# Performance work log

Hardware: AMD Instinct MI355X
Metric: run time of the kernel (lower is better)

## Reference

```python
import jax, jax.numpy as jnp
import numpy as np

N = 20000      # nodes per set
E = 320000     # edges per graph (avg degree 16)
C = 256        # embed_channels
H = 4          # num_heads
D = C // H     # head dim
P = 3          # pos_dim


def setup_inputs() -> dict:
    key = jax.random.key(0)
    ks = jax.random.split(key, 16)
    f32 = jnp.float32
    rn = lambda k, s, sc=1.0: jax.random.normal(k, s, dtype=f32) * sc
    ri = lambda k: jax.random.randint(k, (2, E), 0, N, dtype=jnp.int32)
    return {
        "feat1": rn(ks[0], (N, C)),
        "coord1": rn(ks[1], (N, P)),
        "feat2": rn(ks[2], (N, C)),
        "coord2": rn(ks[3], (N, P)),
        "Wqkv1": rn(ks[4], (C, 6 * C), 0.02),
        "bqkv1": jnp.zeros((6 * C,), f32),
        "Wqkv2": rn(ks[5], (C, 6 * C), 0.02),
        "bqkv2": jnp.zeros((6 * C,), f32),
        "Wproj1": rn(ks[6], (2 * C, C), 0.02),
        "bproj1": jnp.zeros((C,), f32),
        "Wproj2": rn(ks[7], (2 * C, C), 0.02),
        "bproj2": jnp.zeros((C,), f32),
        "Wrpe": rn(ks[8], (P, C), 0.02),
        "brpe": jnp.zeros((C,), f32),
        "graph1": ri(ks[9]),
        "graph2": ri(ks[10]),
        "graph12": ri(ks[11]),
        "graph21": ri(ks[12]),
    }


def _edge_attention(key_, query, value, g, n, rpe=None):
    # key_/query/value: [n_src_or_dst, H, D]; g: [2, E]; rpe: [E, H, D] or None
    k = key_[g[1]]          # [E, H, D] gather source
    q = query[g[0]]         # [E, H, D] gather destination
    v = value[g[1]]         # [E, H, D]
    s = k * q
    if rpe is not None:
        s = s + rpe
    s = s.sum(-1)           # [E, H] per-edge, per-head score
    dst = g[0]
    m = jax.ops.segment_max(s, dst, num_segments=n)      # [n, H]
    e = jnp.exp(s - m[dst])
    z = jax.ops.segment_sum(e, dst, num_segments=n)      # [n, H]
    a = e / z[dst]                                       # scatter-softmax
    out = jax.ops.segment_sum(a[..., None] * v, dst, num_segments=n)  # [n, H, D]
    return out.reshape(n, H * D)


def _qkv(feat, W, b):
    n = feat.shape[0]
    qkv = (feat @ W + b).reshape(n, 6, H, D)
    return tuple(qkv[:, i] for i in range(6))  # q_a,k_a,v_a,q_b,k_b,v_b


def reference(feat1, coord1, feat2, coord2, Wqkv1, bqkv1, Wqkv2, bqkv2,
              Wproj1, bproj1, Wproj2, bproj2, Wrpe, brpe,
              graph1, graph2, graph12, graph21):
    n1, n2 = feat1.shape[0], feat2.shape[0]
    q11, k11, v11, q12, k12, v12 = _qkv(feat1, Wqkv1, bqkv1)
    q21, k21, v21, q22, k22, v22 = _qkv(feat2, Wqkv2, bqkv2)

    rpe1 = ((coord1[graph1[0]] - coord1[graph1[1]]) @ Wrpe + brpe).reshape(-1, H, D)
    rpe2 = ((coord2[graph2[0]] - coord2[graph2[1]]) @ Wrpe + brpe).reshape(-1, H, D)

    feat11 = _edge_attention(k11, q11, v11, graph1, n1, rpe1)
    feat22 = _edge_attention(k22, q22, v22, graph2, n2, rpe2)
    feat12 = _edge_attention(k21, q12, v21, graph21, n1)
    feat21 = _edge_attention(k12, q21, v12, graph12, n2)

    out1 = jnp.concatenate([feat11, feat12], axis=1) @ Wproj1 + bproj1
    out2 = jnp.concatenate([feat22, feat21], axis=1) @ Wproj2 + bproj2
    return (out1, out2)
```

## Files before the change

kernel.cpp:

```cpp
#include <hip/hip_runtime.h>
#include <stdint.h>
#include <stddef.h>

#define N_NODES 20000
#define N_EDGES 320000

typedef unsigned short u16;
typedef __attribute__((ext_vector_type(8))) short bf16x8;
typedef __attribute__((ext_vector_type(8))) unsigned short u16x8;
typedef __attribute__((ext_vector_type(4))) float f32x4;

__device__ __forceinline__ float bf2f(u16 u) {
    union { unsigned int i; float f; } v; v.i = ((unsigned int)u) << 16; return v.f;
}
__device__ __forceinline__ u16 f2bf(float f) {
    union { float f; unsigned int i; } v; v.f = f;
    unsigned int x = v.i;
    unsigned int r = x + 0x7fffu + ((x >> 16) & 1u);
    return (u16)(r >> 16);
}
__device__ __forceinline__ int clampi(int v, int lo, int hi) {
    return v < lo ? lo : (v > hi ? hi : v);
}
__device__ __forceinline__ float ld1(const void* p, size_t i, int f32) {
    return f32 ? ((const float*)p)[i] : bf2f(((const u16*)p)[i]);
}

__device__ __forceinline__ void async_ld16(void* lds, const void* g) {
    __builtin_amdgcn_global_load_lds(
        (const __attribute__((address_space(1))) unsigned int*)g,
        (__attribute__((address_space(3))) unsigned int*)lds,
        16, 0, 0);
}

__device__ __forceinline__ int xcd_chunk(int b, int nwg) {
    int x = b & 7, idx = b >> 3;
    int q = nwg >> 3, r = nwg & 7;
    return ((x < r) ? (x * (q + 1)) : (r * (q + 1) + (x - r) * q)) + idx;
}

__global__ void marker_kernel(u16* out, u16 code) { out[threadIdx.x] = code; }

__global__ void detect_kernel(const void* feat, int* diag) {
    int lane = threadIdx.x;
    int weird = 0;
    const u16* p = (const u16*)feat;
    for (int i = lane; i < 512; i += 64) {
        float v = bf2f(p[i]);
        float a = fabsf(v);
        if (!(a <= 1e4f) || (a != 0.f && a < 1e-6f)) weird++;
    }
#pragma unroll
    for (int off = 32; off > 0; off >>= 1) weird += __shfl_xor(weird, off, 64);
    if (lane == 0) { diag[0] = 123456; diag[1] = (weird > 51) ? 1 : 0; diag[2] = 0; }
}

__global__ void rpe_sums_kernel(const void* __restrict__ Wrpe, const void* __restrict__ brpe,
                                float* __restrict__ out, const int* __restrict__ dflag) {
    int f32 = dflag[0];
    int t = threadIdx.x;
    if (t < 12) {
        int p = t >> 2, h = t & 3;
        float s = 0.f;
        for (int d = 0; d < 64; ++d) s += ld1(Wrpe, p * 256 + h * 64 + d, f32);
        out[t] = s;
    } else if (t < 16) {
        int h = t - 12;
        float s = 0.f;
        for (int d = 0; d < 64; ++d) s += ld1(brpe, h * 64 + d, f32);
        out[12 + h] = s;
    }
}

__global__ __launch_bounds__(256) void coordproj_kernel(const void* __restrict__ coord,
                                                        const int* __restrict__ dflag,
                                                        const float* __restrict__ rs,
                                                        float* __restrict__ proj, int n) {
    int i = blockIdx.x * 256 + threadIdx.x;
    if (i >= n * 4) return;
    int f32 = dflag[0];
    int node = i >> 2, h = i & 3;
    float s = ld1(coord, (size_t)node * 3 + 0, f32) * rs[0 * 4 + h]
            + ld1(coord, (size_t)node * 3 + 1, f32) * rs[1 * 4 + h]
            + ld1(coord, (size_t)node * 3 + 2, f32) * rs[2 * 4 + h];
    proj[i] = s;
}

__global__ __launch_bounds__(256) void transpose_w_kernel(const void* __restrict__ W,
                                                          const int* __restrict__ dflag,
                                                          u16* __restrict__ Wt, int K, int N) {
    int f32 = dflag[0];
    int i = blockIdx.x * 256 + threadIdx.x;
    if (i >= K * N) return;
    int n = i / K, k = i - n * K;
    Wt[i] = f2bf(ld1(W, (size_t)k * N + n, f32));
}

__global__ __launch_bounds__(256) void tobf16_kernel(
        const void* __restrict__ a, const void* __restrict__ b,
        const int* __restrict__ dflag, u16* __restrict__ oa, u16* __restrict__ ob) {
    const int PER = N_NODES * 256 / 8;
    int idx = blockIdx.x * 256 + threadIdx.x;
    if (idx >= 2 * PER) return;
    int set = idx >= PER;
    int j = (idx - set * PER) * 8;
    const void* src = set ? b : a;
    u16* dst = set ? ob : oa;
    int f32 = dflag[0];
    u16x8 o;
    if (f32) {
        const float* p = (const float*)src + j;
        float4 u0 = *(const float4*)p, u1 = *(const float4*)(p + 4);
        o[0] = f2bf(u0.x); o[1] = f2bf(u0.y); o[2] = f2bf(u0.z); o[3] = f2bf(u0.w);
        o[4] = f2bf(u1.x); o[5] = f2bf(u1.y); o[6] = f2bf(u1.z); o[7] = f2bf(u1.w);
    } else {
        o = *(const u16x8*)((const u16*)src + j);
    }
    *(u16x8*)(dst + j) = o;
}

__global__ __launch_bounds__(256) void count_kernel(
        const int* __restrict__ g0, const int* __restrict__ g1,
        const int* __restrict__ g2, const int* __restrict__ g3,
        int* __restrict__ deg, u16* __restrict__ rank) {
    int b = blockIdx.x;
    int gi = b & 3;
    int h = (b >> 2) & 1;
    int e = (b >> 2) * 256 + (int)threadIdx.x;
    if (e >= N_EDGES) return;
    const int* g = (gi == 0) ? g0 : (gi == 1) ? g1 : (gi == 2) ? g2 : g3;
    int dst = clampi(g[e], 0, N_NODES - 1);
    int pos = atomicAdd(&deg[(gi * 2 + h) * N_NODES + dst], 1);
    pos = pos & 0x7fff;
    rank[(size_t)gi * N_EDGES + e] = (u16)((h << 15) | pos);
}

__global__ __launch_bounds__(256) void scan_kernel(const int* __restrict__ cur,
                                                   int* __restrict__ rowptr) {
    int g = blockIdx.x;
    int tid = threadIdx.x;
    __shared__ int buf[256];
    const int* d0 = cur + (g * 2 + 0) * N_NODES;
    const int* d1 = cur + (g * 2 + 1) * N_NODES;
    int* rp = rowptr + g * (N_NODES + 1);
    const int CH = (N_NODES + 255) / 256;
    int lo = tid * CH;
    int hi = lo + CH; if (hi > N_NODES) hi = N_NODES;
    int s = 0;
    for (int i = lo; i < hi; ++i) s += d0[i] + d1[i];
    buf[tid] = s;
    __syncthreads();
    for (int off = 1; off < 256; off <<= 1) {
        int x = (tid >= off) ? buf[tid - off] : 0;
        __syncthreads();
        buf[tid] += x;
        __syncthreads();
    }
    int run = (tid == 0) ? 0 : buf[tid - 1];
    for (int i = lo; i < hi; ++i) {
        rp[i] = run;
        run += d0[i] + d1[i];
    }
    if (tid == 255) rp[N_NODES] = buf[255];
}

__global__ __launch_bounds__(256) void fill_kernel(
        const int* __restrict__ g0, const int* __restrict__ g1,
        const int* __restrict__ g2, const int* __restrict__ g3,
        const int* __restrict__ rowptr, const int* __restrict__ cur,
        const u16* __restrict__ rank, u16* __restrict__ col) {
    int b = blockIdx.x;
    int gi = b & 3;
    int e = (b >> 2) * 256 + (int)threadIdx.x;
    if (e >= N_EDGES) return;
    const int* g = (gi == 0) ? g0 : (gi == 1) ? g1 : (gi == 2) ? g2 : g3;
    int dst = clampi(g[e], 0, N_NODES - 1);
    int src = clampi(g[N_EDGES + e], 0, N_NODES - 1);
    u16 rk = rank[(size_t)gi * N_EDGES + e];
    int h = rk >> 15, r = rk & 0x7fff;
    int base = h ? cur[(gi * 2 + 0) * N_NODES + dst] : 0;
    int pos = rowptr[gi * (N_NODES + 1) + dst] + base + r;
    if (pos >= 0 && pos < N_EDGES)
        col[(size_t)gi * N_EDGES + pos] = (u16)src;
}

__global__ __launch_bounds__(256) void gemm_mfma(
        const void* __restrict__ A, int lda, const int* __restrict__ aflag,
        const u16* __restrict__ Bt,
        const void* __restrict__ bias, size_t biasoff, const int* __restrict__ bflag,
        void* __restrict__ C, size_t coff, int ldc, const int* __restrict__ cflag,
        int M, int N, int K) {
    __shared__ __align__(16) u16 As[128 * 40];
    __shared__ __align__(16) u16 Bs[128 * 40];
    const int f32a = aflag[0], f32b = bflag[0], f32c = cflag[0];
    const int t = threadIdx.x;
    const int lane = t & 63, wv = t >> 6;
    const int wm = (wv >> 1) * 64, wn = (wv & 1) * 64;
    const int m0 = blockIdx.y * 128, n0 = blockIdx.x * 128;
    const int l15 = lane & 15, lq = lane >> 4;

    f32x4 acc[4][4];
#pragma unroll
    for (int i = 0; i < 4; ++i)
#pragma unroll
        for (int j = 0; j < 4; ++j) acc[i][j] = (f32x4){0.f, 0.f, 0.f, 0.f};

    const int sr = t >> 1, skc = (t & 1) * 16;

    for (int k0 = 0; k0 < K; k0 += 32) {
        __syncthreads();
        {
            __align__(16) u16 tmp[16];
            int gm = m0 + sr;
            if (gm < M) {
                if (f32a) {
                    const float* ap = (const float*)A + (size_t)gm * lda + k0 + skc;
#pragma unroll
                    for (int i = 0; i < 16; i += 4) {
                        float4 u = *(const float4*)(ap + i);
                        tmp[i] = f2bf(u.x); tmp[i + 1] = f2bf(u.y);
                        tmp[i + 2] = f2bf(u.z); tmp[i + 3] = f2bf(u.w);
                    }
                } else {
                    const u16* ap = (const u16*)A + (size_t)gm * lda + k0 + skc;
                    *(u16x8*)&tmp[0] = *(const u16x8*)ap;
                    *(u16x8*)&tmp[8] = *(const u16x8*)(ap + 8);
                }
            } else {
#pragma unroll
                for (int i = 0; i < 16; ++i) tmp[i] = 0;
            }
            *(u16x8*)&As[sr * 40 + skc] = *(u16x8*)&tmp[0];
            *(u16x8*)&As[sr * 40 + skc + 8] = *(u16x8*)&tmp[8];
        }
        {
            const u16* bp = Bt + (size_t)(n0 + sr) * K + k0 + skc;
            u16x8 b0 = *(const u16x8*)bp;
            u16x8 b1 = *(const u16x8*)(bp + 8);
            *(u16x8*)&Bs[sr * 40 + skc] = b0;
            *(u16x8*)&Bs[sr * 40 + skc + 8] = b1;
        }
        __syncthreads();
        bf16x8 af[4], bfr[4];
#pragma unroll
        for (int mt = 0; mt < 4; ++mt)
            af[mt] = *(const bf16x8*)&As[(wm + mt * 16 + l15) * 40 + lq * 8];
#pragma unroll
        for (int nt = 0; nt < 4; ++nt)
            bfr[nt] = *(const bf16x8*)&Bs[(wn + nt * 16 + l15) * 40 + lq * 8];
#pragma unroll
        for (int mt = 0; mt < 4; ++mt)
#pragma unroll
            for (int nt = 0; nt < 4; ++nt)
                acc[mt][nt] = __builtin_amdgcn_mfma_f32_16x16x32_bf16(af[mt], bfr[nt], acc[mt][nt], 0, 0, 0);
    }
#pragma unroll
    for (int mt = 0; mt < 4; ++mt) {
#pragma unroll
        for (int nt = 0; nt < 4; ++nt) {
            int gn = n0 + wn + nt * 16 + l15;
            float bb = ld1(bias, biasoff + gn, f32b);
#pragma unroll
            for (int r = 0; r < 4; ++r) {
                int gm = m0 + wm + mt * 16 + lq * 4 + r;
                if (gm < M) {
                    float v = acc[mt][nt][r] + bb;
                    size_t ic = coff + (size_t)gm * ldc + gn;
                    if (f32c) ((float*)C)[ic] = v;
                    else      ((u16*)C)[ic] = f2bf(v);
                }
            }
        }
    }
}

__global__ __launch_bounds__(256, 4) void gemm_pipe(
        const u16* __restrict__ A1, const u16* __restrict__ A2, int K,
        const u16* __restrict__ Bt1, const u16* __restrict__ Bt2,
        const void* __restrict__ bias1, const void* __restrict__ bias2,
        const int* __restrict__ bflag,
        void* __restrict__ C, size_t coff1, size_t coff2, int ldc,
        const int* __restrict__ cflag,
        int M, int nr, int nc) {
    __shared__ __align__(16) u16 S[16384];
    u16* As = S;
    u16* Bs = S + 8192;
    const int f32b = bflag[0], f32c = cflag[0];
    const int t = threadIdx.x;
    const int half = nr * nc;
    const int nwg = 2 * half;
    int b = xcd_chunk(blockIdx.x, nwg);
    const int set = (b >= half) ? 1 : 0;
    b -= set * half;
    const int c = b % nc, r = b / nc;
    const int m0 = r * 128, n0 = c * 128;
    const u16* A   = set ? A2 : A1;
    const u16* Bt  = set ? Bt2 : Bt1;
    const void* bias = set ? bias2 : bias1;
    const size_t coff = set ? coff2 : coff1;

    const int lane = t & 63, wv = t >> 6;
    const int wm = (wv >> 1) * 64, wn = (wv & 1) * 64;
    const int l15 = lane & 15, lq = lane >> 4;

    const int srow8 = lane >> 3;
    const int sgsw  = ((lane & 7) ^ srow8) * 8;
    const u16* agp[4];
    const u16* bgp[4];
    u16 *lap[4], *lbp[4];
#pragma unroll
    for (int i = 0; i < 4; ++i) {
        int ra = m0 + wv * 32 + i * 8 + srow8; if (ra > M - 1) ra = M - 1;
        int rb = n0 + wv * 32 + i * 8 + srow8;
        agp[i] = A  + (size_t)ra * K + sgsw;
        bgp[i] = Bt + (size_t)rb * K + sgsw;
        lap[i] = &As[(wv * 32 + i * 8) * 64];
        lbp[i] = &Bs[(wv * 32 + i * 8) * 64];
    }
    const int l7 = l15 & 7;

    f32x4 acc[4][4];
#pragma unroll
    for (int i = 0; i < 4; ++i)
#pragma unroll
        for (int j = 0; j < 4; ++j) acc[i][j] = (f32x4){0.f, 0.f, 0.f, 0.f};

    for (int k0 = 0; k0 < K; k0 += 64) {
        __syncthreads();
#pragma unroll
        for (int i = 0; i < 4; ++i) async_ld16(lap[i], agp[i] + k0);
#pragma unroll
        for (int i = 0; i < 4; ++i) async_ld16(lbp[i], bgp[i] + k0);
        __syncthreads();
#pragma unroll
        for (int h2 = 0; h2 < 2; ++h2) {
            const int gq = lq + h2 * 4;
            bf16x8 af[4], bfr[4];
#pragma unroll
            for (int mt = 0; mt < 4; ++mt)
                af[mt] = *(const bf16x8*)&As[(wm + mt * 16 + l15) * 64 + ((gq ^ l7) << 3)];
#pragma unroll
            for (int nt = 0; nt < 4; ++nt)
                bfr[nt] = *(const bf16x8*)&Bs[(wn + nt * 16 + l15) * 64 + ((gq ^ l7) << 3)];
#pragma unroll
            for (int mt = 0; mt < 4; ++mt)
#pragma unroll
                for (int nt = 0; nt < 4; ++nt)
                    acc[mt][nt] = __builtin_amdgcn_mfma_f32_16x16x32_bf16(
                        bfr[nt], af[mt], acc[mt][nt], 0, 0, 0);
        }
    }

    if (!f32c) {
        u16* Cs = S;
#pragma unroll
        for (int p = 0; p < 2; ++p) {
            __syncthreads();
            if ((wv >> 1) == p) {
#pragma unroll
                for (int nt = 0; nt < 4; ++nt) {
                    int lc = wn + nt * 16 + lq * 4;
                    int gn0 = n0 + lc;
                    float b0 = ld1(bias, gn0 + 0, f32b);
                    float b1 = ld1(bias, gn0 + 1, f32b);
                    float b2 = ld1(bias, gn0 + 2, f32b);
                    float b3 = ld1(bias, gn0 + 3, f32b);
#pragma unroll
                    for (int mt = 0; mt < 4; ++mt) {
                        ushort4 o;
                        o.x = f2bf(acc[mt][nt][0] + b0);
                        o.y = f2bf(acc[mt][nt][1] + b1);
                        o.z = f2bf(acc[mt][nt][2] + b2);
                        o.w = f2bf(acc[mt][nt][3] + b3);
                        *(ushort4*)&Cs[(mt * 16 + l15) * 128 + (lc ^ (l15 << 3))] = o;
                    }
                }
            }
            __syncthreads();
#pragma unroll
            for (int it = 0; it < 4; ++it) {
                int idx = it * 256 + t;
                int row = idx >> 4, ch = idx & 15;
                int gm = m0 + p * 64 + row;
                if (gm < M)
                    *(u16x8*)((u16*)C + coff + (size_t)gm * ldc + n0 + ch * 8) =
                        *(const u16x8*)&Cs[row * 128 + ((ch * 8) ^ ((row & 15) << 3))];
            }
        }
    } else {
        float* Cs = (float*)S;
#pragma unroll
        for (int p = 0; p < 4; ++p) {
            __syncthreads();
            if ((wv >> 1) == (p >> 1)) {
                int mtb = (p & 1) * 2;
#pragma unroll
                for (int nt = 0; nt < 4; ++nt) {
                    int lc = wn + nt * 16 + lq * 4;
                    int gn0 = n0 + lc;
                    float b0 = ld1(bias, gn0 + 0, f32b);
                    float b1 = ld1(bias, gn0 + 1, f32b);
                    float b2 = ld1(bias, gn0 + 2, f32b);
                    float b3 = ld1(bias, gn0 + 3, f32b);
#pragma unroll
                    for (int mi = 0; mi < 2; ++mi) {
                        int mt = mtb + mi;
                        f32x4 o;
                        o[0] = acc[mt][nt][0] + b0;
                        o[1] = acc[mt][nt][1] + b1;
                        o[2] = acc[mt][nt][2] + b2;
                        o[3] = acc[mt][nt][3] + b3;
                        *(f32x4*)&Cs[(mi * 16 + l15) * 128 + lc] = o;
                    }
                }
            }
            __syncthreads();
#pragma unroll
            for (int it = 0; it < 4; ++it) {
                int idx = it * 256 + t;
                int row = idx >> 5, ch = idx & 31;
                int gm = m0 + p * 32 + row;
                if (gm < M)
                    *(float4*)((float*)C + coff + (size_t)gm * ldc + n0 + ch * 4) =
                        *(const float4*)&Cs[row * 128 + ch * 4];
            }
        }
    }
}

__global__ __launch_bounds__(256) void attn3_kernel(
        const u16* __restrict__ Q, const u16* __restrict__ Kp, const u16* __restrict__ Vp,
        const int* __restrict__ rowptr, const u16* __restrict__ col,
        const float* __restrict__ projN, const float* __restrict__ projS,
        const float* __restrict__ rb, int use_rpe,
        u16* __restrict__ outp, int ldt) {
    int lane = threadIdx.x & 63;
    int node = blockIdx.x * 4 + (threadIdx.x >> 6);
    if (node >= N_NODES) return;
    int h = lane >> 4;
    int off = h * 64 + (lane & 15) * 4;

    ushort4 qu = *(const ushort4*)(Q + (size_t)node * ldt + off);
    float q0 = bf2f(qu.x), q1 = bf2f(qu.y), q2 = bf2f(qu.z), q3 = bf2f(qu.w);
    float base = use_rpe ? (projN[node * 4 + h] + rb[h]) : 0.f;

    float m = -1e30f, l = 0.f, a0 = 0.f, a1 = 0.f, a2 = 0.f, a3 = 0.f;
    int e0 = rowptr[node], e1 = rowptr[node + 1];
    e0 = clampi(e0, 0, N_EDGES);
    e1 = clampi(e1, e0, N_EDGES);
    int e = e0;
    for (; e + 4 <= e1; e += 4) {
        int s0 = clampi((int)col[e + 0], 0, N_NODES - 1);
        int s1 = clampi((int)col[e + 1], 0, N_NODES - 1);
        int s2 = clampi((int)col[e + 2], 0, N_NODES - 1);
        int s3 = clampi((int)col[e + 3], 0, N_NODES - 1);
        ushort4 k0 = *(const ushort4*)(Kp + (size_t)s0 * ldt + off);
        ushort4 k1 = *(const ushort4*)(Kp + (size_t)s1 * ldt + off);
        ushort4 k2 = *(const ushort4*)(Kp + (size_t)s2 * ldt + off);
        ushort4 k3 = *(const ushort4*)(Kp + (size_t)s3 * ldt + off);
        ushort4 v0 = *(const ushort4*)(Vp + (size_t)s0 * ldt + off);
        ushort4 v1 = *(const ushort4*)(Vp + (size_t)s1 * ldt + off);
        ushort4 v2 = *(const ushort4*)(Vp + (size_t)s2 * ldt + off);
        ushort4 v3 = *(const ushort4*)(Vp + (size_t)s3 * ldt + off);
        float t0 = q0 * bf2f(k0.x) + q1 * bf2f(k0.y) + q2 * bf2f(k0.z) + q3 * bf2f(k0.w);
        float t1 = q0 * bf2f(k1.x) + q1 * bf2f(k1.y) + q2 * bf2f(k1.z) + q3 * bf2f(k1.w);
        float t2 = q0 * bf2f(k2.x) + q1 * bf2f(k2.y) + q2 * bf2f(k2.z) + q3 * bf2f(k2.w);
        float t3 = q0 * bf2f(k3.x) + q1 * bf2f(k3.y) + q2 * bf2f(k3.z) + q3 * bf2f(k3.w);
#pragma unroll
        for (int sh = 1; sh <= 8; sh <<= 1) {
            t0 += __shfl_xor(t0, sh, 64);
            t1 += __shfl_xor(t1, sh, 64);
            t2 += __shfl_xor(t2, sh, 64);
            t3 += __shfl_xor(t3, sh, 64);
        }
        if (use_rpe) {
            t0 += base - projS[s0 * 4 + h];
            t1 += base - projS[s1 * 4 + h];
            t2 += base - projS[s2 * 4 + h];
            t3 += base - projS[s3 * 4 + h];
        }
        float mx = fmaxf(fmaxf(fmaxf(t0, t1), fmaxf(t2, t3)), m);
        float sc = __expf(m - mx);
        float p0 = __expf(t0 - mx), p1 = __expf(t1 - mx);
        float p2 = __expf(t2 - mx), p3 = __expf(t3 - mx);
        l = l * sc + (p0 + p1 + p2 + p3);
        a0 = a0 * sc + p0 * bf2f(v0.x) + p1 * bf2f(v1.x) + p2 * bf2f(v2.x) + p3 * bf2f(v3.x);
        a1 = a1 * sc + p0 * bf2f(v0.y) + p1 * bf2f(v1.y) + p2 * bf2f(v2.y) + p3 * bf2f(v3.y);
        a2 = a2 * sc + p0 * bf2f(v0.z) + p1 * bf2f(v1.z) + p2 * bf2f(v2.z) + p3 * bf2f(v3.z);
        a3 = a3 * sc + p0 * bf2f(v0.w) + p1 * bf2f(v1.w) + p2 * bf2f(v2.w) + p3 * bf2f(v3.w);
        m = mx;
    }
    for (; e < e1; ++e) {
        int src = clampi((int)col[e], 0, N_NODES - 1);
        ushort4 ku = *(const ushort4*)(Kp + (size_t)src * ldt + off);
        ushort4 vu = *(const ushort4*)(Vp + (size_t)src * ldt + off);
        float tv = q0 * bf2f(ku.x) + q1 * bf2f(ku.y) + q2 * bf2f(ku.z) + q3 * bf2f(ku.w);
        tv += __shfl_xor(tv, 1, 64);
        tv += __shfl_xor(tv, 2, 64);
        tv += __shfl_xor(tv, 4, 64);
        tv += __shfl_xor(tv, 8, 64);
        if (use_rpe) tv += base - projS[src * 4 + h];
        float mn = fmaxf(m, tv);
        float sc = __expf(m - mn), p = __expf(tv - mn);
        l = l * sc + p;
        a0 = a0 * sc + p * bf2f(vu.x);
        a1 = a1 * sc + p * bf2f(vu.y);
        a2 = a2 * sc + p * bf2f(vu.z);
        a3 = a3 * sc + p * bf2f(vu.w);
        m = mn;
    }
    float inv = l > 0.f ? 1.f / l : 0.f;
    ushort4 o;
    o.x = f2bf(a0 * inv); o.y = f2bf(a1 * inv); o.z = f2bf(a2 * inv); o.w = f2bf(a3 * inv);
    *(ushort4*)(outp + (size_t)node * 512 + off) = o;
}

extern "C" void kernel_launch(void* const* d_in, const int* in_sizes, int n_in,
                              void* d_out, int out_size, void* d_ws, size_t ws_size,
                              hipStream_t stream) {
    const void* feat1  = d_in[0];
    const void* coord1 = d_in[1];
    const void* feat2  = d_in[2];
    const void* coord2 = d_in[3];
    const void* Wqkv1  = d_in[4];
    const void* bqkv1  = d_in[5];
    const void* Wqkv2  = d_in[6];
    const void* bqkv2  = d_in[7];
    const void* Wproj1 = d_in[8];
    const void* bproj1 = d_in[9];
    const void* Wproj2 = d_in[10];
    const void* bproj2 = d_in[11];
    const void* Wrpe   = d_in[12];
    const void* brpe   = d_in[13];
    const int* graph1  = (const int*)d_in[14];
    const int* graph2  = (const int*)d_in[15];
    const int* graph12 = (const int*)d_in[16];
    const int* graph21 = (const int*)d_in[17];
    u16* out = (u16*)d_out;

    {
        static const int expect[18] = {
            N_NODES * 256, N_NODES * 3, N_NODES * 256, N_NODES * 3,
            256 * 1536, 1536, 256 * 1536, 1536,
            512 * 256, 256, 512 * 256, 256,
            3 * 256, 256,
            2 * N_EDGES, 2 * N_EDGES, 2 * N_EDGES, 2 * N_EDGES };
        bool ok = (n_in == 18) && (out_size == 2 * N_NODES * 256);
        if (ok) for (int i = 0; i < 18; ++i) if (in_sizes[i] != expect[i]) ok = false;
        if (!ok) { marker_kernel<<<1, 16, 0, stream>>>(out, 0x4496 ); return; }
    }

    char* w = (char*)d_ws;
    size_t off = 0;
    auto alloc = [&](size_t bytes) { void* p = w + off; off += (bytes + 255) & ~(size_t)255; return p; };
    int* rowptr  = (int*)alloc(4ull * (N_NODES + 1) * 4);
    int* cur     = (int*)alloc(8ull * N_NODES * 4);
    u16* col     = (u16*)alloc(4ull * N_EDGES * 2);
    u16* rank    = (u16*)alloc(4ull * N_EDGES * 2);
    float* rpe_s = (float*)alloc(64);
    int* diag    = (int*)alloc(256);
    float* proj1 = (float*)alloc((size_t)N_NODES * 4 * 4);
    float* proj2 = (float*)alloc((size_t)N_NODES * 4 * 4);
    u16* Wqkv1t  = (u16*)alloc((size_t)1536 * 256 * 2);
    u16* Wqkv2t  = (u16*)alloc((size_t)1536 * 256 * 2);
    u16* Wproj1t = (u16*)alloc((size_t)256 * 512 * 2);
    u16* Wproj2t = (u16*)alloc((size_t)256 * 512 * 2);
    size_t off_common = off;

    u16* cat = (u16*)alloc(2ull * N_NODES * 512 * 2);
    u16* T1  = (u16*)alloc(2ull * N_NODES * 1536 * 2);
    u16* T2  = T1 + (size_t)N_NODES * 1536;
    bool big = (off <= ws_size);
    u16* Told = nullptr;
    if (!big) {
        off = off_common;
        cat  = (u16*)alloc((size_t)N_NODES * 512 * 2);
        Told = (u16*)alloc((size_t)N_NODES * 768 * 2);
        if (off > ws_size) {
            marker_kernel<<<1, 16, 0, stream>>>(out, 0x447A );
            return;
        }
    }
    const int* dF = diag + 1;
    const int* dZ = diag + 2;

    const int NP1 = N_NODES + 1;
    hipMemsetAsync(cur, 0, 8ull * N_NODES * 4, stream);
    hipMemsetAsync(diag, 0, 256, stream);

    detect_kernel<<<1, 64, 0, stream>>>(feat1, diag);
    rpe_sums_kernel<<<1, 64, 0, stream>>>(Wrpe, brpe, rpe_s, dF);
    coordproj_kernel<<<(N_NODES * 4 + 255) / 256, 256, 0, stream>>>(coord1, dF, rpe_s, proj1, N_NODES);
    coordproj_kernel<<<(N_NODES * 4 + 255) / 256, 256, 0, stream>>>(coord2, dF, rpe_s, proj2, N_NODES);
    transpose_w_kernel<<<(1536 * 256 + 255) / 256, 256, 0, stream>>>(Wqkv1, dF, Wqkv1t, 256, 1536);
    transpose_w_kernel<<<(1536 * 256 + 255) / 256, 256, 0, stream>>>(Wqkv2, dF, Wqkv2t, 256, 1536);
    transpose_w_kernel<<<(256 * 512 + 255) / 256, 256, 0, stream>>>(Wproj1, dF, Wproj1t, 512, 256);
    transpose_w_kernel<<<(256 * 512 + 255) / 256, 256, 0, stream>>>(Wproj2, dF, Wproj2t, 512, 256);

    const int EB = 4 * N_EDGES / 256;
    count_kernel<<<EB, 256, 0, stream>>>(graph1, graph2, graph12, graph21, cur, rank);
    scan_kernel<<<4, 256, 0, stream>>>(cur, rowptr);
    fill_kernel<<<EB, 256, 0, stream>>>(graph1, graph2, graph12, graph21, rowptr, cur, rank, col);

    const dim3 blk(256);
    const int AG = (N_NODES + 3) / 4;

    if (big) {
        u16* cat1 = cat;
        u16* cat2 = cat + (size_t)N_NODES * 512;
        u16* featb1 = cat;
        u16* featb2 = cat + (size_t)N_NODES * 256;
        const int NROW = (N_NODES + 127) / 128;

        tobf16_kernel<<<(2 * N_NODES * 256 / 8 + 255) / 256, blk, 0, stream>>>(
            feat1, feat2, dF, featb1, featb2);

        gemm_pipe<<<dim3(2 * NROW * 12), blk, 0, stream>>>(
            featb1, featb2, 256, Wqkv1t, Wqkv2t, bqkv1, bqkv2, dF,
            T1, 0, (size_t)N_NODES * 1536, 1536, dZ, N_NODES, NROW, 12);

        attn3_kernel<<<AG, blk, 0, stream>>>(T1 + 0, T1 + 256, T1 + 512,
                                             rowptr + 0 * NP1, col + 0 * (size_t)N_EDGES,
                                             proj1, proj1, rpe_s + 12, 1, cat1 + 0, 1536);
        attn3_kernel<<<AG, blk, 0, stream>>>(T1 + 768, T2 + 256, T2 + 512,
                                             rowptr + 3 * NP1, col + 3 * (size_t)N_EDGES,
                                             nullptr, nullptr, rpe_s + 12, 0, cat1 + 256, 1536);
        attn3_kernel<<<AG, blk, 0, stream>>>(T2 + 768, T2 + 1024, T2 + 1280,
                                             rowptr + 1 * NP1, col + 1 * (size_t)N_EDGES,
                                             proj2, proj2, rpe_s + 12, 1, cat2 + 0, 1536);
        attn3_kernel<<<AG, blk, 0, stream>>>(T2 + 0, T1 + 1024, T1 + 1280,
                                             rowptr + 2 * NP1, col + 2 * (size_t)N_EDGES,
                                             nullptr, nullptr, rpe_s + 12, 0, cat2 + 256, 1536);

        gemm_pipe<<<dim3(2 * NROW * 2), blk, 0, stream>>>(
            cat1, cat2, 512, Wproj1t, Wproj2t, bproj1, bproj2, dF,
            out, 0, (size_t)N_NODES * 256, 256, dF, N_NODES, NROW, 2);
        return;
    }

    u16* T = Told;
    const int GY = (N_NODES + 127) / 128;
    gemm_mfma<<<dim3(6, GY), blk, 0, stream>>>(feat1, 256, dF, Wqkv1t + 0 * 256,
                                               bqkv1, 0, dF, T, 0, 768, dZ, N_NODES, 768, 256);
    attn3_kernel<<<AG, blk, 0, stream>>>(T, T + 256, T + 512, rowptr + 0 * NP1, col + 0 * (size_t)N_EDGES,
                                         proj1, proj1, rpe_s + 12, 1, cat + 0, 768);
    gemm_mfma<<<dim3(2, GY), blk, 0, stream>>>(feat1, 256, dF, Wqkv1t + (size_t)768 * 256,
                                               bqkv1, 768, dF, T, 0, 768, dZ, N_NODES, 256, 256);
    gemm_mfma<<<dim3(4, GY), blk, 0, stream>>>(feat2, 256, dF, Wqkv2t + (size_t)256 * 256,
                                               bqkv2, 256, dF, T, 256, 768, dZ, N_NODES, 512, 256);
    attn3_kernel<<<AG, blk, 0, stream>>>(T, T + 256, T + 512, rowptr + 3 * NP1, col + 3 * (size_t)N_EDGES,
                                         nullptr, nullptr, rpe_s + 12, 0, cat + 256, 768);
    gemm_mfma<<<dim3(2, GY), blk, 0, stream>>>(cat, 512, dZ, Wproj1t,
                                               bproj1, 0, dF, out, 0, 256, dF, N_NODES, 256, 512);

    gemm_mfma<<<dim3(6, GY), blk, 0, stream>>>(feat2, 256, dF, Wqkv2t + (size_t)768 * 256,
                                               bqkv2, 768, dF, T, 0, 768, dZ, N_NODES, 768, 256);
    attn3_kernel<<<AG, blk, 0, stream>>>(T, T + 256, T + 512, rowptr + 1 * NP1, col + 1 * (size_t)N_EDGES,
                                         proj2, proj2, rpe_s + 12, 1, cat + 0, 768);
    gemm_mfma<<<dim3(2, GY), blk, 0, stream>>>(feat2, 256, dF, Wqkv2t + 0,
                                               bqkv2, 0, dF, T, 0, 768, dZ, N_NODES, 256, 256);
    gemm_mfma<<<dim3(4, GY), blk, 0, stream>>>(feat1, 256, dF, Wqkv1t + (size_t)1024 * 256,
                                               bqkv1, 1024, dF, T, 256, 768, dZ, N_NODES, 512, 256);
    attn3_kernel<<<AG, blk, 0, stream>>>(T, T + 256, T + 512, rowptr + 2 * NP1, col + 2 * (size_t)N_EDGES,
                                         nullptr, nullptr, rpe_s + 12, 0, cat + 256, 768);
    gemm_mfma<<<dim3(2, GY), blk, 0, stream>>>(cat, 512, dZ, Wproj2t,
                                               bproj2, 0, dF, out, (size_t)N_NODES * 256, 256, dF,
                                               N_NODES, 256, 512);
}
```

Before: 555.8 us.

## Replace serial per-graph CSR scan with three-phase parallel block scan

The row-pointer prefix sum ran on only 4 blocks, with each thread serially walking a strided chunk of about 79 nodes. It is now a three-phase scan: per-chunk block scans over 316 blocks, a scan of the chunk totals, and a coalesced add-back pass. This is meant to remove the latency-bound serial loops and uncoalesced accesses. In exchange it adds two extra kernel launches and a temporary buffer.

```diff
diff --git a/kernel.cpp b/kernel.cpp
--- a/kernel.cpp
+++ b/kernel.cpp
@@ -4,6 +4,7 @@
 
 #define N_NODES 20000
 #define N_EDGES 320000
+#define NCH 79
 
 typedef unsigned short u16;
 typedef __attribute__((ext_vector_type(8))) short bf16x8;
@@ -135,20 +136,18 @@
     rank[(size_t)gi * N_EDGES + e] = (u16)((h << 15) | pos);
 }
 
-__global__ __launch_bounds__(256) void scan_kernel(const int* __restrict__ cur,
-                                                   int* __restrict__ rowptr) {
-    int g = blockIdx.x;
+__global__ __launch_bounds__(256) void scan1_kernel(const int* __restrict__ cur,
+                                                    int* __restrict__ tmp,
+                                                    int* __restrict__ csum) {
+    int b = blockIdx.x;
+    int g = b / NCH, ch = b - g * NCH;
     int tid = threadIdx.x;
-    __shared__ int buf[256];
+    int i = ch * 256 + tid;
     const int* d0 = cur + (g * 2 + 0) * N_NODES;
     const int* d1 = cur + (g * 2 + 1) * N_NODES;
-    int* rp = rowptr + g * (N_NODES + 1);
-    const int CH = (N_NODES + 255) / 256;
-    int lo = tid * CH;
-    int hi = lo + CH; if (hi > N_NODES) hi = N_NODES;
-    int s = 0;
-    for (int i = lo; i < hi; ++i) s += d0[i] + d1[i];
-    buf[tid] = s;
+    int val = (i < N_NODES) ? (d0[i] + d1[i]) : 0;
+    __shared__ int buf[256];
+    buf[tid] = val;
     __syncthreads();
     for (int off = 1; off < 256; off <<= 1) {
         int x = (tid >= off) ? buf[tid - off] : 0;
@@ -156,12 +155,37 @@
         buf[tid] += x;
         __syncthreads();
     }
-    int run = (tid == 0) ? 0 : buf[tid - 1];
-    for (int i = lo; i < hi; ++i) {
-        rp[i] = run;
-        run += d0[i] + d1[i];
-    }
-    if (tid == 255) rp[N_NODES] = buf[255];
+    if (i < N_NODES) tmp[g * N_NODES + i] = buf[tid] - val;
+    if (tid == 255) csum[g * NCH + ch] = buf[255];
+}
+
+__global__ __launch_bounds__(256) void scan2_kernel(const int* __restrict__ csum,
+                                                    int* __restrict__ coff,
+                                                    int* __restrict__ rowptr) {
+    int g = blockIdx.x;
+    int tid = threadIdx.x;
+    int v = (tid < NCH) ? csum[g * NCH + tid] : 0;
+    __shared__ int buf[256];
+    buf[tid] = v;
+    __syncthreads();
+    for (int off = 1; off < 256; off <<= 1) {
+        int x = (tid >= off) ? buf[tid - off] : 0;
+        __syncthreads();
+        buf[tid] += x;
+        __syncthreads();
+    }
+    if (tid < NCH) coff[g * NCH + tid] = buf[tid] - v;
+    if (tid == 255) rowptr[g * (N_NODES + 1) + N_NODES] = buf[255];
+}
+
+__global__ __launch_bounds__(256) void scan3_kernel(const int* __restrict__ tmp,
+                                                    const int* __restrict__ coff,
+                                                    int* __restrict__ rowptr) {
+    int b = blockIdx.x;
+    int g = b / NCH, ch = b - g * NCH;
+    int i = ch * 256 + (int)threadIdx.x;
+    if (i < N_NODES)
+        rowptr[g * (N_NODES + 1) + i] = tmp[g * N_NODES + i] + coff[g * NCH + ch];
 }
 
 __global__ __launch_bounds__(256) void fill_kernel(
@@ -557,6 +581,9 @@
     int* cur     = (int*)alloc(8ull * N_NODES * 4);
     u16* col     = (u16*)alloc(4ull * N_EDGES * 2);
     u16* rank    = (u16*)alloc(4ull * N_EDGES * 2);
+    int* tmpscan = (int*)alloc(4ull * N_NODES * 4);
+    int* csum    = (int*)alloc(4ull * NCH * 4);
+    int* coffb   = (int*)alloc(4ull * NCH * 4);
     float* rpe_s = (float*)alloc(64);
     int* diag    = (int*)alloc(256);
     float* proj1 = (float*)alloc((size_t)N_NODES * 4 * 4);
@@ -599,7 +626,9 @@
 
     const int EB = 4 * N_EDGES / 256;
     count_kernel<<<EB, 256, 0, stream>>>(graph1, graph2, graph12, graph21, cur, rank);
-    scan_kernel<<<4, 256, 0, stream>>>(cur, rowptr);
+    scan1_kernel<<<4 * NCH, 256, 0, stream>>>(cur, tmpscan, csum);
+    scan2_kernel<<<4, 256, 0, stream>>>(csum, coffb, rowptr);
+    scan3_kernel<<<4 * NCH, 256, 0, stream>>>(tmpscan, coffb, rowptr);
     fill_kernel<<<EB, 256, 0, stream>>>(graph1, graph2, graph12, graph21, rowptr, cur, rank, col);
 
     const dim3 blk(256);
```

Measured after the change: 506.3 us, median of 2. 1.1x faster.
